# Kernel optimization log

Hardware: AMD Instinct MI355X
Metric: run time of the kernel (lower is better)

Reference implementation:

```python
import jax, jax.numpy as jnp
import numpy as np

N_NODES = 20000
N_EDGES = 320000
HIDDEN = 64
M = 8            # extra per-node sample axis implied by Linear2's (N, B, M) layout
IN_DIM = 1
OUT_DIM = 1
N_LAYERS = 5
BN_EPS = 1e-5


def setup_inputs() -> dict:
    key = jax.random.key(0)
    ks = jax.random.split(key, 10)
    x = jax.random.normal(ks[0], (N_NODES, IN_DIM, M), dtype=jnp.float32)
    edge_index = jax.random.randint(ks[1], (2, N_EDGES), 0, N_NODES, dtype=jnp.int64)
    batch = jnp.zeros((N_NODES,), dtype=jnp.int64)
    s = 0.1
    w1_0 = jax.random.normal(ks[2], (HIDDEN, IN_DIM), dtype=jnp.float32) * s
    w1 = jax.random.normal(ks[3], (N_LAYERS - 1, HIDDEN, HIDDEN), dtype=jnp.float32) * s
    b1 = jax.random.normal(ks[4], (N_LAYERS, HIDDEN), dtype=jnp.float32) * s
    w2 = jax.random.normal(ks[5], (N_LAYERS, HIDDEN, HIDDEN), dtype=jnp.float32) * s
    b2 = jax.random.normal(ks[6], (N_LAYERS, HIDDEN), dtype=jnp.float32) * s
    gamma = jnp.ones((N_LAYERS, HIDDEN), dtype=jnp.float32)
    beta = jnp.zeros((N_LAYERS, HIDDEN), dtype=jnp.float32)
    w_out = jax.random.normal(ks[7], (OUT_DIM, HIDDEN), dtype=jnp.float32) * s
    b_out = jnp.zeros((OUT_DIM,), dtype=jnp.float32)
    return {"x": x, "edge_index": edge_index, "batch": batch,
            "w1_0": w1_0, "w1": w1, "b1": b1, "w2": w2, "b2": b2,
            "gamma": gamma, "beta": beta, "w_out": w_out, "b_out": b_out}


def reference(x, edge_index, batch, w1_0, w1, b1, w2, b2, gamma, beta, w_out, b_out):
    src, dst = edge_index[0], edge_index[1]
    n = x.shape[0]
    h = x  # [N, C, M]
    for i in range(N_LAYERS):
        # GINConv (eps=0): nn(x + sum of neighbor features scattered by dst)
        agg = jax.ops.segment_sum(h[src], dst, num_segments=n)
        z = h + agg
        W1 = w1_0 if i == 0 else w1[i - 1]
        # Linear2 applies the linear over the channel axis (axis 1)
        z = jnp.einsum('ncm,oc->nom', z, W1) + b1[i][None, :, None]
        z = jax.nn.relu(z)
        z = jnp.einsum('ncm,oc->nom', z, w2[i]) + b2[i][None, :, None]
        z = jax.nn.relu(z)
        # BatchNorm1d over (N, C, M): per-channel stats over N and M (training-mode batch stats)
        mean = z.mean(axis=(0, 2), keepdims=True)
        var = z.var(axis=(0, 2), keepdims=True)
        z = (z - mean) * jax.lax.rsqrt(var + BN_EPS)
        z = z * gamma[i][None, :, None] + beta[i][None, :, None]
        # Dropout(0.5) treated as identity (eval behavior, deterministic reference)
        h = z
    # global mean pool with batch of all zeros -> single graph
    pooled = h.mean(axis=0, keepdims=True)          # [1, H, M]
    pooled = jnp.transpose(pooled, (0, 2, 1))        # [1, M, H]
    out = jax.nn.sigmoid(jnp.einsum('bmh,oh->bmo', pooled, w_out) + b_out)
    return out  # [1, M, OUT_DIM]
```

## Files before the change

### kernel.cpp

```cpp
#include <hip/hip_runtime.h>

#define N_NODES 20000
#define N_EDGES 320000
#define HID 64
#define MDIM 8
#define ROW 512
#define NM 160000.0f
#define NCHUNK 79
#define NSHADOW 16
#define ZSTRIDE 72

typedef unsigned int uint;
typedef unsigned char uchar;
typedef unsigned short ushort;
typedef __attribute__((ext_vector_type(8))) short bf16x8;
typedef __attribute__((ext_vector_type(4))) float f32x4;
typedef __attribute__((ext_vector_type(2))) float f32x2;

union U4B8 { uint4 u; bf16x8 b; };

__device__ __forceinline__ float bflo(uint u) { return __uint_as_float(u << 16); }
__device__ __forceinline__ float bfhi(uint u) { return __uint_as_float(u & 0xffff0000u); }
__device__ __forceinline__ uint f2bf(float f) {
    uint u = __float_as_uint(f);
    return (u + 0x7fffu + ((u >> 16) & 1u)) >> 16;
}
__device__ __forceinline__ uint pack2(float lo, float hi) { return f2bf(lo) | (f2bf(hi) << 16); }
__device__ __forceinline__ uint2 pkfp8(uint4 pk) {
    int lo = 0, hi = 0;
    lo = __builtin_amdgcn_cvt_pk_fp8_f32(bflo(pk.x), bfhi(pk.x), lo, false);
    lo = __builtin_amdgcn_cvt_pk_fp8_f32(bflo(pk.y), bfhi(pk.y), lo, true);
    hi = __builtin_amdgcn_cvt_pk_fp8_f32(bflo(pk.z), bfhi(pk.z), hi, false);
    hi = __builtin_amdgcn_cvt_pk_fp8_f32(bflo(pk.w), bfhi(pk.w), hi, true);
    uint2 r; r.x = (uint)lo; r.y = (uint)hi; return r;
}

__global__ __launch_bounds__(256) void k_hist(const int* __restrict__ dst, int* __restrict__ deg) {
    int e = blockIdx.x * 256 + threadIdx.x;
    if (e < N_EDGES) atomicAdd(&deg[dst[e]], 1);
}

__global__ __launch_bounds__(256) void k_csum(const int* __restrict__ deg, int* __restrict__ csum) {
    __shared__ int r[256];
    int t = threadIdx.x, i = blockIdx.x * 256 + t;
    r[t] = (i < N_NODES) ? deg[i] : 0;
    __syncthreads();
    for (int s = 128; s > 0; s >>= 1) { if (t < s) r[t] += r[t + s]; __syncthreads(); }
    if (t == 0) csum[blockIdx.x] = r[0];
}

__global__ __launch_bounds__(128) void k_cscan(const int* __restrict__ csum, int* __restrict__ chunkoff) {
    __shared__ int s[128];
    int t = threadIdx.x;
    s[t] = (t < NCHUNK) ? csum[t] : 0;
    __syncthreads();
    if (t == 0) { int run = 0; for (int j = 0; j < NCHUNK; ++j) { int x = s[j]; s[j] = run; run += x; } }
    __syncthreads();
    if (t < NCHUNK) chunkoff[t] = s[t];
}

__global__ __launch_bounds__(256) void k_chunkscan(const int* __restrict__ deg, const int* __restrict__ chunkoff,
                                                   int* __restrict__ offs) {
    __shared__ int sd[256];
    int t = threadIdx.x, i = blockIdx.x * 256 + t;
    int v = (i < N_NODES) ? deg[i] : 0;
    sd[t] = v;
    __syncthreads();
    for (int off = 1; off < 256; off <<= 1) {
        int x = (t >= off) ? sd[t - off] : 0;
        __syncthreads();
        sd[t] += x;
        __syncthreads();
    }
    if (i < N_NODES) offs[i] = sd[t] - v + chunkoff[blockIdx.x];
}

__global__ __launch_bounds__(256) void k_fill(const int* __restrict__ src, const int* __restrict__ dst,
                                              const int* __restrict__ offs, int* __restrict__ cursor,
                                              int* __restrict__ esrc) {
    int e = blockIdx.x * 256 + threadIdx.x;
    if (e < N_EDGES) {
        int d = dst[e];
        int p = atomicAdd(&cursor[d], 1);
        esrc[offs[d] + p] = src[e];
    }
}

__global__ __launch_bounds__(256) void k_prep(const float* __restrict__ w1, const float* __restrict__ w2,
                                              uint4* __restrict__ wfrag) {
    int id = blockIdx.x * 256 + threadIdx.x;
    if (id >= 4608) return;
    const float* W;
    int s;
    if (id < 4096) {
        int layer = id >> 10;
        int rem = id & 1023;
        int which = rem >> 9;
        s = rem & 511;
        W = which ? &w2[(size_t)(layer + 1) * 4096] : &w1[(size_t)layer * 4096];
    } else {
        s = id - 4096;
        W = w2;
    }
    int f = s >> 6, l = s & 63;
    int o = (f >> 1) * 16 + (l & 15);
    int c0 = (f & 1) * 32 + (l >> 4) * 8;
    const float* p = &W[o * 64 + c0];
    uint4 a;
    a.x = pack2(p[0], p[1]); a.y = pack2(p[2], p[3]);
    a.z = pack2(p[4], p[5]); a.w = pack2(p[6], p[7]);
    wfrag[id] = a;
}

__global__ __launch_bounds__(256) void k_layer0(const float* __restrict__ x, const int* __restrict__ offs,
                                                const int* __restrict__ deg, const int* __restrict__ esrc,
                                                const float* __restrict__ W10, const float* __restrict__ B1,
                                                const uint4* __restrict__ w2f0, const float* __restrict__ B2,
                                                uchar* __restrict__ zout8, float* __restrict__ shadow) {
    __shared__ uint4 w2s[512];
    __shared__ __align__(16) ushort zbuf[128 * ZSTRIDE];
    int tid = threadIdx.x;
    for (int s2 = tid; s2 < 512; s2 += 256) w2s[s2] = w2f0[s2];
    __syncthreads();
    int w = tid >> 6, t = tid & 63;
    int n0 = blockIdx.x * 16 + w * 4;
    int g = t >> 3, m = t & 7;
    float zin0v[4];
    #pragma unroll
    for (int i = 0; i < 4; ++i) {
        int n = n0 + i;
        int off = offs[n], dg = deg[n];
        float acc = (t < 8) ? x[n * 8 + t] : 0.f;
        for (int base = 0; base < dg; base += 8) {
            int k = base + g;
            float v = 0.f;
            if (k < dg) { int nb = esrc[off + k]; v = x[(size_t)nb * 8 + m]; }
            acc += v;
        }
        acc += __shfl_xor(acc, 8);
        acc += __shfl_xor(acc, 16);
        acc += __shfl_xor(acc, 32);
        zin0v[i] = acc;
    }
    bf16x8 bfr[2][2];
    #pragma unroll
    for (int q2 = 0; q2 < 2; ++q2) {
        int kb = q2 * 32 + (t >> 4) * 8;
        float4 wA = *(const float4*)&W10[kb];
        float4 wB = *(const float4*)&W10[kb + 4];
        float4 bA = *(const float4*)&B1[kb];
        float4 bB = *(const float4*)&B1[kb + 4];
        #pragma unroll
        for (int tau = 0; tau < 2; ++tau) {
            float zv = zin0v[tau * 2 + ((t & 15) >> 3)];
            U4B8 u;
            u.u.x = pack2(fmaxf(fmaf(wA.x, zv, bA.x), 0.f), fmaxf(fmaf(wA.y, zv, bA.y), 0.f));
            u.u.y = pack2(fmaxf(fmaf(wA.z, zv, bA.z), 0.f), fmaxf(fmaf(wA.w, zv, bA.w), 0.f));
            u.u.z = pack2(fmaxf(fmaf(wB.x, zv, bB.x), 0.f), fmaxf(fmaf(wB.y, zv, bB.y), 0.f));
            u.u.w = pack2(fmaxf(fmaf(wB.z, zv, bB.z), 0.f), fmaxf(fmaf(wB.w, zv, bB.w), 0.f));
            bfr[q2][tau] = u.b;
        }
    }
    f32x4 acc[4][2];
    #pragma unroll
    for (int o4 = 0; o4 < 4; ++o4) {
        float4 bv = *(const float4*)&B2[o4 * 16 + (t >> 4) * 4];
        #pragma unroll
        for (int tau = 0; tau < 2; ++tau) acc[o4][tau] = (f32x4){bv.x, bv.y, bv.z, bv.w};
    }
    #pragma unroll
    for (int o4 = 0; o4 < 4; ++o4)
        #pragma unroll
        for (int q2 = 0; q2 < 2; ++q2) {
            U4B8 a; a.u = w2s[(o4 * 2 + q2) * 64 + t];
            #pragma unroll
            for (int tau = 0; tau < 2; ++tau)
                acc[o4][tau] = __builtin_amdgcn_mfma_f32_16x16x32_bf16(a.b, bfr[q2][tau], acc[o4][tau], 0, 0, 0);
        }
    #pragma unroll
    for (int o4 = 0; o4 < 4; ++o4)
        #pragma unroll
        for (int tau = 0; tau < 2; ++tau) {
            acc[o4][tau][0] = fmaxf(acc[o4][tau][0], 0.f);
            acc[o4][tau][1] = fmaxf(acc[o4][tau][1], 0.f);
            acc[o4][tau][2] = fmaxf(acc[o4][tau][2], 0.f);
            acc[o4][tau][3] = fmaxf(acc[o4][tau][3], 0.f);
        }
    int sid = (blockIdx.x & (NSHADOW - 1)) * 128;
    #pragma unroll
    for (int o4 = 0; o4 < 4; ++o4)
        #pragma unroll
        for (int r = 0; r < 4; ++r) {
            float x0 = acc[o4][0][r], x1 = acc[o4][1][r];
            float sv = x0 + x1;
            float ssv = x0 * x0 + x1 * x1;
            sv += __shfl_xor(sv, 1);  ssv += __shfl_xor(ssv, 1);
            sv += __shfl_xor(sv, 2);  ssv += __shfl_xor(ssv, 2);
            sv += __shfl_xor(sv, 4);  ssv += __shfl_xor(ssv, 4);
            sv += __shfl_xor(sv, 8);  ssv += __shfl_xor(ssv, 8);
            if ((t & 15) == o4 * 4 + r) {
                int ch = o4 * 16 + (t >> 4) * 4 + r;
                atomicAdd(&shadow[sid + ch], sv);
                atomicAdd(&shadow[sid + 64 + ch], ssv);
            }
        }
    #pragma unroll
    for (int o4 = 0; o4 < 4; ++o4)
        #pragma unroll
        for (int tau = 0; tau < 2; ++tau) {
            uint* p = (uint*)&zbuf[(w * 32 + tau * 16 + (t & 15)) * ZSTRIDE + o4 * 16 + (t >> 4) * 4];
            p[0] = pack2(acc[o4][tau][0], acc[o4][tau][1]);
            p[1] = pack2(acc[o4][tau][2], acc[o4][tau][3]);
        }
    #pragma unroll
    for (int i = 0; i < 4; ++i) {
        uint4 pk = *(const uint4*)&zbuf[(w * 32 + i * 8 + (t >> 3)) * ZSTRIDE + (t & 7) * 8];
        ((uint2*)(zout8 + (size_t)(n0 + i) * ROW))[t] = pkfp8(pk);
    }
}

#define PAIRLD(rr, jj) do { \
    int nb_l = __builtin_amdgcn_readlane(idx, (jj)); \
    int nb_h = __builtin_amdgcn_readlane(idx, (jj) + 1); \
    int nb_ = hi ? nb_h : nb_l; \
    rr = ((const uint4*)(zprev8 + (size_t)nb_ * ROW))[q]; \
} while (0)

#define ACC16(rr) do { \
    f32x2 p_; \
    p_ = __builtin_amdgcn_cvt_pk_f32_fp8((int)rr.x, false); s0  += p_.x; s1  += p_.y; \
    p_ = __builtin_amdgcn_cvt_pk_f32_fp8((int)rr.x, true);  s2  += p_.x; s3  += p_.y; \
    p_ = __builtin_amdgcn_cvt_pk_f32_fp8((int)rr.y, false); s4  += p_.x; s5  += p_.y; \
    p_ = __builtin_amdgcn_cvt_pk_f32_fp8((int)rr.y, true);  s6  += p_.x; s7  += p_.y; \
    p_ = __builtin_amdgcn_cvt_pk_f32_fp8((int)rr.z, false); s8  += p_.x; s9  += p_.y; \
    p_ = __builtin_amdgcn_cvt_pk_f32_fp8((int)rr.z, true);  s10 += p_.x; s11 += p_.y; \
    p_ = __builtin_amdgcn_cvt_pk_f32_fp8((int)rr.w, false); s12 += p_.x; s13 += p_.y; \
    p_ = __builtin_amdgcn_cvt_pk_f32_fp8((int)rr.w, true);  s14 += p_.x; s15 += p_.y; \
} while (0)

__global__ __launch_bounds__(256) void k_layer(const uchar* __restrict__ zprev8,
                                               const float* __restrict__ shadow_prev,
                                               const float* __restrict__ gammaP, const float* __restrict__ betaP,
                                               const int* __restrict__ offs, const int* __restrict__ deg,
                                               const int* __restrict__ esrc,
                                               const uint4* __restrict__ w1f, const float* __restrict__ B1,
                                               const uint4* __restrict__ w2f, const float* __restrict__ B2,
                                               uchar* __restrict__ zout8, float* __restrict__ shadow) {
    __shared__ __align__(16) ushort zbuf[128 * ZSTRIDE];
    __shared__ float red[128];
    __shared__ __align__(16) float abl[128];
    int tid = threadIdx.x;
    int w = tid >> 6, t = tid & 63;
    int n0 = blockIdx.x * 16 + w * 4;
    int q = t & 31;
    int hi = t >> 5;
    int offv[4], dgv[4], idxv[4];
    #pragma unroll
    for (int i = 0; i < 4; ++i) { offv[i] = offs[n0 + i]; dgv[i] = deg[n0 + i]; }
    #pragma unroll
    for (int i = 0; i < 4; ++i) idxv[i] = (t < dgv[i]) ? esrc[offv[i] + t] : 0;
    if (tid < 128) {
        float s = 0.f;
        #pragma unroll
        for (int j = 0; j < NSHADOW; ++j) s += shadow_prev[j * 128 + tid];
        red[tid] = s;
    }
    __syncthreads();
    if (tid < 64) {
        float mean = red[tid] * (1.f / NM);
        float var = red[64 + tid] * (1.f / NM) - mean * mean;
        float a = gammaP[tid] * rsqrtf(var + 1e-5f);
        abl[tid] = a;
        abl[64 + tid] = betaP[tid] - mean * a;
    }
    __syncthreads();
    const float4* abp = (const float4*)abl;
    #pragma unroll
    for (int i = 0; i < 4; ++i) {
        int n = n0 + i;
        int off = offv[i], dg = dgv[i];
        float s0 = 0.f, s1 = 0.f, s2 = 0.f, s3 = 0.f, s4 = 0.f, s5 = 0.f, s6 = 0.f, s7 = 0.f;
        float s8 = 0.f, s9 = 0.f, s10 = 0.f, s11 = 0.f, s12 = 0.f, s13 = 0.f, s14 = 0.f, s15 = 0.f;
        for (int base = 0; base < dg; base += 64) {
            int cnt = dg - base; if (cnt > 64) cnt = 64;
            int idx = base ? ((t < cnt) ? esrc[off + base + t] : 0) : idxv[i];
            int j = 0;
            for (; j + 7 < cnt; j += 8) {
                uint4 r0, r1, r2, r3;
                PAIRLD(r0, j); PAIRLD(r1, j + 2); PAIRLD(r2, j + 4); PAIRLD(r3, j + 6);
                ACC16(r0); ACC16(r1); ACC16(r2); ACC16(r3);
            }
            for (; j + 1 < cnt; j += 2) {
                uint4 r0;
                PAIRLD(r0, j);
                ACC16(r0);
            }
            if (j < cnt) {
                int nb = __builtin_amdgcn_readlane(idx, j);
                if (!hi) {
                    uint4 r0 = ((const uint4*)(zprev8 + (size_t)nb * ROW))[q];
                    ACC16(r0);
                }
            }
        }
        float u, r0, r1, r2, r3, r4, r5, r6, r7;
        u = hi ? s0 : s8;   r0 = (hi ? s8  : s0) + __shfl_xor(u, 32);
        u = hi ? s1 : s9;   r1 = (hi ? s9  : s1) + __shfl_xor(u, 32);
        u = hi ? s2 : s10;  r2 = (hi ? s10 : s2) + __shfl_xor(u, 32);
        u = hi ? s3 : s11;  r3 = (hi ? s11 : s3) + __shfl_xor(u, 32);
        u = hi ? s4 : s12;  r4 = (hi ? s12 : s4) + __shfl_xor(u, 32);
        u = hi ? s5 : s13;  r5 = (hi ? s13 : s5) + __shfl_xor(u, 32);
        u = hi ? s6 : s14;  r6 = (hi ? s14 : s6) + __shfl_xor(u, 32);
        u = hi ? s7 : s15;  r7 = (hi ? s15 : s7) + __shfl_xor(u, 32);
        {
            uint2 sv = ((const uint2*)(zprev8 + (size_t)n * ROW))[q * 2 + hi];
            f32x2 p_;
            p_ = __builtin_amdgcn_cvt_pk_f32_fp8((int)sv.x, false); r0 += p_.x; r1 += p_.y;
            p_ = __builtin_amdgcn_cvt_pk_f32_fp8((int)sv.x, true);  r2 += p_.x; r3 += p_.y;
            p_ = __builtin_amdgcn_cvt_pk_f32_fp8((int)sv.y, false); r4 += p_.x; r5 += p_.y;
            p_ = __builtin_amdgcn_cvt_pk_f32_fp8((int)sv.y, true);  r6 += p_.x; r7 += p_.y;
        }
        int c4 = (q & 3) * 4 + hi * 2;
        float4 Af0 = abp[c4], Af1 = abp[c4 + 1];
        float4 Bf0 = abp[16 + c4], Bf1 = abp[16 + c4 + 1];
        float dp1 = (float)(dg + 1);
        uint4 pk;
        pk.x = pack2(fmaf(Af0.x, r0, Bf0.x * dp1), fmaf(Af0.y, r1, Bf0.y * dp1));
        pk.y = pack2(fmaf(Af0.z, r2, Bf0.z * dp1), fmaf(Af0.w, r3, Bf0.w * dp1));
        pk.z = pack2(fmaf(Af1.x, r4, Bf1.x * dp1), fmaf(Af1.y, r5, Bf1.y * dp1));
        pk.w = pack2(fmaf(Af1.z, r6, Bf1.z * dp1), fmaf(Af1.w, r7, Bf1.w * dp1));
        *(uint4*)&zbuf[(w * 32 + i * 8 + (q >> 2)) * ZSTRIDE + (q & 3) * 16 + hi * 8] = pk;
    }
    bf16x8 bfr[2][2];
    #pragma unroll
    for (int tau = 0; tau < 2; ++tau)
        #pragma unroll
        for (int q2 = 0; q2 < 2; ++q2) {
            U4B8 u;
            u.u = *(const uint4*)&zbuf[(w * 32 + tau * 16 + (t & 15)) * ZSTRIDE + q2 * 32 + (t >> 4) * 8];
            bfr[q2][tau] = u.b;
        }
    f32x4 acc[4][2];
    #pragma unroll
    for (int o4 = 0; o4 < 4; ++o4) {
        float4 bv = *(const float4*)&B1[o4 * 16 + (t >> 4) * 4];
        #pragma unroll
        for (int tau = 0; tau < 2; ++tau) acc[o4][tau] = (f32x4){bv.x, bv.y, bv.z, bv.w};
    }
    #pragma unroll
    for (int o4 = 0; o4 < 4; ++o4)
        #pragma unroll
        for (int q2 = 0; q2 < 2; ++q2) {
            U4B8 a; a.u = w1f[(o4 * 2 + q2) * 64 + t];
            #pragma unroll
            for (int tau = 0; tau < 2; ++tau)
                acc[o4][tau] = __builtin_amdgcn_mfma_f32_16x16x32_bf16(a.b, bfr[q2][tau], acc[o4][tau], 0, 0, 0);
        }
    #pragma unroll
    for (int o4 = 0; o4 < 4; ++o4)
        #pragma unroll
        for (int tau = 0; tau < 2; ++tau) {
            f32x4 v = acc[o4][tau];
            float h0 = fmaxf(v[0], 0.f), h1 = fmaxf(v[1], 0.f), h2 = fmaxf(v[2], 0.f), h3 = fmaxf(v[3], 0.f);
            uint* p = (uint*)&zbuf[(w * 32 + tau * 16 + (t & 15)) * ZSTRIDE + o4 * 16 + (t >> 4) * 4];
            p[0] = pack2(h0, h1); p[1] = pack2(h2, h3);
        }
    #pragma unroll
    for (int tau = 0; tau < 2; ++tau)
        #pragma unroll
        for (int q2 = 0; q2 < 2; ++q2) {
            U4B8 u;
            u.u = *(const uint4*)&zbuf[(w * 32 + tau * 16 + (t & 15)) * ZSTRIDE + q2 * 32 + (t >> 4) * 8];
            bfr[q2][tau] = u.b;
        }
    #pragma unroll
    for (int o4 = 0; o4 < 4; ++o4) {
        float4 bv = *(const float4*)&B2[o4 * 16 + (t >> 4) * 4];
        #pragma unroll
        for (int tau = 0; tau < 2; ++tau) acc[o4][tau] = (f32x4){bv.x, bv.y, bv.z, bv.w};
    }
    #pragma unroll
    for (int o4 = 0; o4 < 4; ++o4)
        #pragma unroll
        for (int q2 = 0; q2 < 2; ++q2) {
            U4B8 a; a.u = w2f[(o4 * 2 + q2) * 64 + t];
            #pragma unroll
            for (int tau = 0; tau < 2; ++tau)
                acc[o4][tau] = __builtin_amdgcn_mfma_f32_16x16x32_bf16(a.b, bfr[q2][tau], acc[o4][tau], 0, 0, 0);
        }
    #pragma unroll
    for (int o4 = 0; o4 < 4; ++o4)
        #pragma unroll
        for (int tau = 0; tau < 2; ++tau) {
            acc[o4][tau][0] = fmaxf(acc[o4][tau][0], 0.f);
            acc[o4][tau][1] = fmaxf(acc[o4][tau][1], 0.f);
            acc[o4][tau][2] = fmaxf(acc[o4][tau][2], 0.f);
            acc[o4][tau][3] = fmaxf(acc[o4][tau][3], 0.f);
        }
    int sid = (blockIdx.x & (NSHADOW - 1)) * 128;
    #pragma unroll
    for (int o4 = 0; o4 < 4; ++o4)
        #pragma unroll
        for (int r = 0; r < 4; ++r) {
            float x0 = acc[o4][0][r], x1 = acc[o4][1][r];
            float sv = x0 + x1;
            float ssv = x0 * x0 + x1 * x1;
            sv += __shfl_xor(sv, 1);  ssv += __shfl_xor(ssv, 1);
            sv += __shfl_xor(sv, 2);  ssv += __shfl_xor(ssv, 2);
            sv += __shfl_xor(sv, 4);  ssv += __shfl_xor(ssv, 4);
            sv += __shfl_xor(sv, 8);  ssv += __shfl_xor(ssv, 8);
            if ((t & 15) == o4 * 4 + r) {
                int ch = o4 * 16 + (t >> 4) * 4 + r;
                atomicAdd(&shadow[sid + ch], sv);
                atomicAdd(&shadow[sid + 64 + ch], ssv);
            }
        }
    #pragma unroll
    for (int o4 = 0; o4 < 4; ++o4)
        #pragma unroll
        for (int tau = 0; tau < 2; ++tau) {
            uint* p = (uint*)&zbuf[(w * 32 + tau * 16 + (t & 15)) * ZSTRIDE + o4 * 16 + (t >> 4) * 4];
            p[0] = pack2(acc[o4][tau][0], acc[o4][tau][1]);
            p[1] = pack2(acc[o4][tau][2], acc[o4][tau][3]);
        }
    #pragma unroll
    for (int i = 0; i < 4; ++i) {
        uint4 pk = *(const uint4*)&zbuf[(w * 32 + i * 8 + (t >> 3)) * ZSTRIDE + (t & 7) * 8];
        ((uint2*)(zout8 + (size_t)(n0 + i) * ROW))[t] = pkfp8(pk);
    }
}

__global__ __launch_bounds__(256) void k_pool(const uint* __restrict__ z8, float* __restrict__ pool) {
    int t = blockIdx.x * 256 + threadIdx.x;
    float s0 = 0.f, s1 = 0.f, s2 = 0.f, s3 = 0.f;
    for (int u = t; u < N_NODES * ROW / 4; u += 65536) {
        uint v = z8[u];
        f32x2 p0 = __builtin_amdgcn_cvt_pk_f32_fp8((int)v, false);
        f32x2 p1 = __builtin_amdgcn_cvt_pk_f32_fp8((int)v, true);
        s0 += p0.x; s1 += p0.y; s2 += p1.x; s3 += p1.y;
    }
    int k4 = t & 127;
    atomicAdd(&pool[k4 * 4 + 0], s0);
    atomicAdd(&pool[k4 * 4 + 1], s1);
    atomicAdd(&pool[k4 * 4 + 2], s2);
    atomicAdd(&pool[k4 * 4 + 3], s3);
}

__global__ __launch_bounds__(64) void k_out(const float* __restrict__ pool, const float* __restrict__ shadow4,
                                            const float* __restrict__ gamma4, const float* __restrict__ beta4,
                                            const float* __restrict__ wout, const float* __restrict__ bout,
                                            float* __restrict__ out) {
    int c = threadIdx.x;
    float s = 0.f, ss = 0.f;
    #pragma unroll
    for (int j = 0; j < NSHADOW; ++j) { s += shadow4[j * 128 + c]; ss += shadow4[j * 128 + 64 + c]; }
    float mean = s * (1.f / NM);
    float var = ss * (1.f / NM) - mean * mean;
    float a = gamma4[c] * rsqrtf(var + 1e-5f);
    float b = beta4[c] - mean * a;
    float wv = wout[c];
    for (int m = 0; m < 8; ++m) {
        float v = wv * (a * pool[m * 64 + c] * (1.f / N_NODES) + b);
        for (int off = 32; off > 0; off >>= 1) v += __shfl_down(v, off);
        if (c == 0) out[m] = 1.f / (1.f + expf(-(v + bout[0])));
    }
}

extern "C" void kernel_launch(void* const* d_in, const int* in_sizes, int n_in,
                              void* d_out, int out_size, void* d_ws, size_t ws_size,
                              hipStream_t stream) {
    const float* x     = (const float*)d_in[0];
    const int*   ei    = (const int*)d_in[1];
    const int*   srcp  = ei;
    const int*   dstp  = ei + N_EDGES;
    const float* w1_0  = (const float*)d_in[3];
    const float* w1    = (const float*)d_in[4];
    const float* b1    = (const float*)d_in[5];
    const float* w2    = (const float*)d_in[6];
    const float* b2    = (const float*)d_in[7];
    const float* gamma = (const float*)d_in[8];
    const float* beta  = (const float*)d_in[9];
    const float* wout  = (const float*)d_in[10];
    const float* bout  = (const float*)d_in[11];
    float* out = (float*)d_out;

    char* ws = (char*)d_ws;
    size_t off = 0;
    auto alloc = [&](size_t bytes) -> void* {
        void* p = ws + off;
        off = (off + bytes + 255) & ~(size_t)255;
        return p;
    };
    uchar* zA8   = (uchar*)alloc((size_t)N_NODES * ROW);
    uchar* zB8   = (uchar*)alloc((size_t)N_NODES * ROW);
    uint4* wfrag = (uint4*)alloc(4608 * 16);
    int* deg      = (int*)alloc(N_NODES * 4);
    int* cursor   = (int*)alloc(N_NODES * 4);
    float* shadow = (float*)alloc(5 * NSHADOW * 128 * 4);
    float* pool   = (float*)alloc(512 * 4);
    size_t zero_bytes = (size_t)((char*)pool - (char*)deg) + 512 * 4;
    int* offs     = (int*)alloc(N_NODES * 4);
    int* esrc     = (int*)alloc(N_EDGES * 4);
    int* csum     = (int*)alloc(NCHUNK * 4);
    int* chunkoff = (int*)alloc(NCHUNK * 4);

    hipMemsetAsync(deg, 0, zero_bytes, stream);

    k_hist<<<(N_EDGES + 255) / 256, 256, 0, stream>>>(dstp, deg);
    k_csum<<<NCHUNK, 256, 0, stream>>>(deg, csum);
    k_cscan<<<1, 128, 0, stream>>>(csum, chunkoff);
    k_chunkscan<<<NCHUNK, 256, 0, stream>>>(deg, chunkoff, offs);
    k_fill<<<(N_EDGES + 255) / 256, 256, 0, stream>>>(srcp, dstp, offs, cursor, esrc);
    k_prep<<<18, 256, 0, stream>>>(w1, w2, wfrag);

    k_layer0<<<N_NODES / 16, 256, 0, stream>>>(x, offs, deg, esrc, w1_0, b1, wfrag + 4096, b2,
                                               zA8, shadow);

    const uchar* zin8 = zA8;
    uchar* zo8 = zB8;
    for (int i = 1; i <= 4; ++i) {
        k_layer<<<N_NODES / 16, 256, 0, stream>>>(zin8,
                                                  shadow + (size_t)(i - 1) * NSHADOW * 128,
                                                  gamma + (i - 1) * 64, beta + (i - 1) * 64,
                                                  offs, deg, esrc,
                                                  wfrag + (size_t)(i - 1) * 1024, b1 + i * 64,
                                                  wfrag + (size_t)(i - 1) * 1024 + 512, b2 + i * 64,
                                                  zo8,
                                                  shadow + (size_t)i * NSHADOW * 128);
        const uchar* t8 = zin8; zin8 = zo8; zo8 = (uchar*)t8;
    }

    k_pool<<<256, 256, 0, stream>>>((const uint*)zA8, pool);
    k_out<<<1, 64, 0, stream>>>(pool, shadow + 4 * NSHADOW * 128, gamma + 256, beta + 256, wout, bout, out);
}
```

Measured before the change: 492.6 us.

## Pad CSR neighbor lists to multiples of 16 with zero node; single-wave layer blocks

Each node's CSR segment is padded to a multiple of 16 entries filled with a dummy zero-row node, so the gather loop runs in fixed 16-neighbor steps with no remainder paths. k_layer also becomes a 64-thread single-wave block with four nodes per block, and the self-row load is hoisted to the start of the kernel. The aim is to remove tail branching and raise the number of independent loads in flight. In exchange the kernel does up to 15 extra dummy gathers per node (about 50% more with an average degree of 16), needs an extra padding kernel and memsets, and recomputes the BN statistics in every small block.

```diff
diff --git a/kernel.cpp b/kernel.cpp
--- a/kernel.cpp
+++ b/kernel.cpp
@@ -9,6 +9,8 @@
 #define NCHUNK 79
 #define NSHADOW 16
 #define ZSTRIDE 72
+#define ZERO_NODE N_NODES
+#define ESRC_CAP 640000
 
 typedef unsigned int uint;
 typedef unsigned char uchar;
@@ -43,7 +45,7 @@
 __global__ __launch_bounds__(256) void k_csum(const int* __restrict__ deg, int* __restrict__ csum) {
     __shared__ int r[256];
     int t = threadIdx.x, i = blockIdx.x * 256 + t;
-    r[t] = (i < N_NODES) ? deg[i] : 0;
+    r[t] = (i < N_NODES) ? ((deg[i] + 15) & ~15) : 0;
     __syncthreads();
     for (int s = 128; s > 0; s >>= 1) { if (t < s) r[t] += r[t + s]; __syncthreads(); }
     if (t == 0) csum[blockIdx.x] = r[0];
@@ -63,7 +65,7 @@
                                                    int* __restrict__ offs) {
     __shared__ int sd[256];
     int t = threadIdx.x, i = blockIdx.x * 256 + t;
-    int v = (i < N_NODES) ? deg[i] : 0;
+    int v = (i < N_NODES) ? ((deg[i] + 15) & ~15) : 0;
     sd[t] = v;
     __syncthreads();
     for (int off = 1; off < 256; off <<= 1) {
@@ -84,6 +86,16 @@
         int p = atomicAdd(&cursor[d], 1);
         esrc[offs[d] + p] = src[e];
     }
+}
+
+__global__ __launch_bounds__(256) void k_pad(const int* __restrict__ deg, const int* __restrict__ offs,
+                                             int* __restrict__ esrc) {
+    int id = blockIdx.x * 256 + threadIdx.x;
+    if (id >= N_NODES * 16) return;
+    int n = id >> 4, s = id & 15;
+    int dg = deg[n], pdg = (dg + 15) & ~15;
+    int p = dg + s;
+    if (p < pdg) esrc[offs[n] + p] = ZERO_NODE;
 }
 
 __global__ __launch_bounds__(256) void k_prep(const float* __restrict__ w1, const float* __restrict__ w2,
@@ -238,69 +250,61 @@
     p_ = __builtin_amdgcn_cvt_pk_f32_fp8((int)rr.w, true);  s14 += p_.x; s15 += p_.y; \
 } while (0)
 
-__global__ __launch_bounds__(256) void k_layer(const uchar* __restrict__ zprev8,
-                                               const float* __restrict__ shadow_prev,
-                                               const float* __restrict__ gammaP, const float* __restrict__ betaP,
-                                               const int* __restrict__ offs, const int* __restrict__ deg,
-                                               const int* __restrict__ esrc,
-                                               const uint4* __restrict__ w1f, const float* __restrict__ B1,
-                                               const uint4* __restrict__ w2f, const float* __restrict__ B2,
-                                               uchar* __restrict__ zout8, float* __restrict__ shadow) {
-    __shared__ __align__(16) ushort zbuf[128 * ZSTRIDE];
-    __shared__ float red[128];
+__global__ __launch_bounds__(64, 4) void k_layer(const uchar* __restrict__ zprev8,
+                                                 const float* __restrict__ shadow_prev,
+                                                 const float* __restrict__ gammaP, const float* __restrict__ betaP,
+                                                 const int* __restrict__ offs, const int* __restrict__ deg,
+                                                 const int* __restrict__ esrc,
+                                                 const uint4* __restrict__ w1f, const float* __restrict__ B1,
+                                                 const uint4* __restrict__ w2f, const float* __restrict__ B2,
+                                                 uchar* __restrict__ zout8, float* __restrict__ shadow) {
+    __shared__ __align__(16) ushort zbuf[32 * ZSTRIDE];
     __shared__ __align__(16) float abl[128];
-    int tid = threadIdx.x;
-    int w = tid >> 6, t = tid & 63;
-    int n0 = blockIdx.x * 16 + w * 4;
+    int t = threadIdx.x;
+    int n0 = blockIdx.x * 4;
     int q = t & 31;
     int hi = t >> 5;
-    int offv[4], dgv[4], idxv[4];
-    #pragma unroll
-    for (int i = 0; i < 4; ++i) { offv[i] = offs[n0 + i]; dgv[i] = deg[n0 + i]; }
-    #pragma unroll
-    for (int i = 0; i < 4; ++i) idxv[i] = (t < dgv[i]) ? esrc[offv[i] + t] : 0;
-    if (tid < 128) {
-        float s = 0.f;
-        #pragma unroll
-        for (int j = 0; j < NSHADOW; ++j) s += shadow_prev[j * 128 + tid];
-        red[tid] = s;
-    }
-    __syncthreads();
-    if (tid < 64) {
-        float mean = red[tid] * (1.f / NM);
-        float var = red[64 + tid] * (1.f / NM) - mean * mean;
-        float a = gammaP[tid] * rsqrtf(var + 1e-5f);
-        abl[tid] = a;
-        abl[64 + tid] = betaP[tid] - mean * a;
+    int offv[4], dgv[4], pdgv[4], idxv[4];
+    uint2 selfv[4];
+    #pragma unroll
+    for (int i = 0; i < 4; ++i) {
+        offv[i] = offs[n0 + i];
+        dgv[i] = deg[n0 + i];
+        pdgv[i] = (dgv[i] + 15) & ~15;
+    }
+    #pragma unroll
+    for (int i = 0; i < 4; ++i) idxv[i] = (t < pdgv[i]) ? esrc[offv[i] + t] : 0;
+    #pragma unroll
+    for (int i = 0; i < 4; ++i) selfv[i] = ((const uint2*)(zprev8 + (size_t)(n0 + i) * ROW))[q * 2 + hi];
+    {
+        float s = 0.f, ss = 0.f;
+        #pragma unroll
+        for (int j = 0; j < NSHADOW; ++j) {
+            s  += shadow_prev[j * 128 + t];
+            ss += shadow_prev[j * 128 + 64 + t];
+        }
+        float mean = s * (1.f / NM);
+        float var = ss * (1.f / NM) - mean * mean;
+        float a = gammaP[t] * rsqrtf(var + 1e-5f);
+        abl[t] = a;
+        abl[64 + t] = betaP[t] - mean * a;
     }
     __syncthreads();
     const float4* abp = (const float4*)abl;
     #pragma unroll
     for (int i = 0; i < 4; ++i) {
-        int n = n0 + i;
-        int off = offv[i], dg = dgv[i];
+        int off = offv[i], dg = dgv[i], pdg = pdgv[i];
         float s0 = 0.f, s1 = 0.f, s2 = 0.f, s3 = 0.f, s4 = 0.f, s5 = 0.f, s6 = 0.f, s7 = 0.f;
         float s8 = 0.f, s9 = 0.f, s10 = 0.f, s11 = 0.f, s12 = 0.f, s13 = 0.f, s14 = 0.f, s15 = 0.f;
-        for (int base = 0; base < dg; base += 64) {
-            int cnt = dg - base; if (cnt > 64) cnt = 64;
+        for (int base = 0; base < pdg; base += 64) {
+            int cnt = pdg - base; if (cnt > 64) cnt = 64;
             int idx = base ? ((t < cnt) ? esrc[off + base + t] : 0) : idxv[i];
-            int j = 0;
-            for (; j + 7 < cnt; j += 8) {
-                uint4 r0, r1, r2, r3;
-                PAIRLD(r0, j); PAIRLD(r1, j + 2); PAIRLD(r2, j + 4); PAIRLD(r3, j + 6);
+            for (int j = 0; j < cnt; j += 16) {
+                uint4 r0, r1, r2, r3, r4, r5, r6, r7;
+                PAIRLD(r0, j);      PAIRLD(r1, j + 2);  PAIRLD(r2, j + 4);  PAIRLD(r3, j + 6);
+                PAIRLD(r4, j + 8);  PAIRLD(r5, j + 10); PAIRLD(r6, j + 12); PAIRLD(r7, j + 14);
                 ACC16(r0); ACC16(r1); ACC16(r2); ACC16(r3);
-            }
-            for (; j + 1 < cnt; j += 2) {
-                uint4 r0;
-                PAIRLD(r0, j);
-                ACC16(r0);
-            }
-            if (j < cnt) {
-                int nb = __builtin_amdgcn_readlane(idx, j);
-                if (!hi) {
-                    uint4 r0 = ((const uint4*)(zprev8 + (size_t)nb * ROW))[q];
-                    ACC16(r0);
-                }
+                ACC16(r4); ACC16(r5); ACC16(r6); ACC16(r7);
             }
         }
         float u, r0, r1, r2, r3, r4, r5, r6, r7;
@@ -313,7 +317,7 @@
         u = hi ? s6 : s14;  r6 = (hi ? s14 : s6) + __shfl_xor(u, 32);
         u = hi ? s7 : s15;  r7 = (hi ? s15 : s7) + __shfl_xor(u, 32);
         {
-            uint2 sv = ((const uint2*)(zprev8 + (size_t)n * ROW))[q * 2 + hi];
+            uint2 sv = selfv[i];
             f32x2 p_;
             p_ = __builtin_amdgcn_cvt_pk_f32_fp8((int)sv.x, false); r0 += p_.x; r1 += p_.y;
             p_ = __builtin_amdgcn_cvt_pk_f32_fp8((int)sv.x, true);  r2 += p_.x; r3 += p_.y;
@@ -329,7 +333,7 @@
         pk.y = pack2(fmaf(Af0.z, r2, Bf0.z * dp1), fmaf(Af0.w, r3, Bf0.w * dp1));
         pk.z = pack2(fmaf(Af1.x, r4, Bf1.x * dp1), fmaf(Af1.y, r5, Bf1.y * dp1));
         pk.w = pack2(fmaf(Af1.z, r6, Bf1.z * dp1), fmaf(Af1.w, r7, Bf1.w * dp1));
-        *(uint4*)&zbuf[(w * 32 + i * 8 + (q >> 2)) * ZSTRIDE + (q & 3) * 16 + hi * 8] = pk;
+        *(uint4*)&zbuf[(i * 8 + (q >> 2)) * ZSTRIDE + (q & 3) * 16 + hi * 8] = pk;
     }
     bf16x8 bfr[2][2];
     #pragma unroll
@@ -337,7 +341,7 @@
         #pragma unroll
         for (int q2 = 0; q2 < 2; ++q2) {
             U4B8 u;
-            u.u = *(const uint4*)&zbuf[(w * 32 + tau * 16 + (t & 15)) * ZSTRIDE + q2 * 32 + (t >> 4) * 8];
+            u.u = *(const uint4*)&zbuf[(tau * 16 + (t & 15)) * ZSTRIDE + q2 * 32 + (t >> 4) * 8];
             bfr[q2][tau] = u.b;
         }
     f32x4 acc[4][2];
@@ -362,7 +366,7 @@
         for (int tau = 0; tau < 2; ++tau) {
             f32x4 v = acc[o4][tau];
             float h0 = fmaxf(v[0], 0.f), h1 = fmaxf(v[1], 0.f), h2 = fmaxf(v[2], 0.f), h3 = fmaxf(v[3], 0.f);
-            uint* p = (uint*)&zbuf[(w * 32 + tau * 16 + (t & 15)) * ZSTRIDE + o4 * 16 + (t >> 4) * 4];
+            uint* p = (uint*)&zbuf[(tau * 16 + (t & 15)) * ZSTRIDE + o4 * 16 + (t >> 4) * 4];
             p[0] = pack2(h0, h1); p[1] = pack2(h2, h3);
         }
     #pragma unroll
@@ -370,7 +374,7 @@
         #pragma unroll
         for (int q2 = 0; q2 < 2; ++q2) {
             U4B8 u;
-            u.u = *(const uint4*)&zbuf[(w * 32 + tau * 16 + (t & 15)) * ZSTRIDE + q2 * 32 + (t >> 4) * 8];
+            u.u = *(const uint4*)&zbuf[(tau * 16 + (t & 15)) * ZSTRIDE + q2 * 32 + (t >> 4) * 8];
             bfr[q2][tau] = u.b;
         }
     #pragma unroll
@@ -419,13 +423,13 @@
     for (int o4 = 0; o4 < 4; ++o4)
         #pragma unroll
         for (int tau = 0; tau < 2; ++tau) {
-            uint* p = (uint*)&zbuf[(w * 32 + tau * 16 + (t & 15)) * ZSTRIDE + o4 * 16 + (t >> 4) * 4];
+            uint* p = (uint*)&zbuf[(tau * 16 + (t & 15)) * ZSTRIDE + o4 * 16 + (t >> 4) * 4];
             p[0] = pack2(acc[o4][tau][0], acc[o4][tau][1]);
             p[1] = pack2(acc[o4][tau][2], acc[o4][tau][3]);
         }
     #pragma unroll
     for (int i = 0; i < 4; ++i) {
-        uint4 pk = *(const uint4*)&zbuf[(w * 32 + i * 8 + (t >> 3)) * ZSTRIDE + (t & 7) * 8];
+        uint4 pk = *(const uint4*)&zbuf[(i * 8 + (t >> 3)) * ZSTRIDE + (t & 7) * 8];
         ((uint2*)(zout8 + (size_t)(n0 + i) * ROW))[t] = pkfp8(pk);
     }
 }
@@ -491,8 +495,8 @@
         off = (off + bytes + 255) & ~(size_t)255;
         return p;
     };
-    uchar* zA8   = (uchar*)alloc((size_t)N_NODES * ROW);
-    uchar* zB8   = (uchar*)alloc((size_t)N_NODES * ROW);
+    uchar* zA8   = (uchar*)alloc((size_t)(N_NODES + 1) * ROW);
+    uchar* zB8   = (uchar*)alloc((size_t)(N_NODES + 1) * ROW);
     uint4* wfrag = (uint4*)alloc(4608 * 16);
     int* deg      = (int*)alloc(N_NODES * 4);
     int* cursor   = (int*)alloc(N_NODES * 4);
@@ -500,17 +504,20 @@
     float* pool   = (float*)alloc(512 * 4);
     size_t zero_bytes = (size_t)((char*)pool - (char*)deg) + 512 * 4;
     int* offs     = (int*)alloc(N_NODES * 4);
-    int* esrc     = (int*)alloc(N_EDGES * 4);
+    int* esrc     = (int*)alloc(ESRC_CAP * 4);
     int* csum     = (int*)alloc(NCHUNK * 4);
     int* chunkoff = (int*)alloc(NCHUNK * 4);
 
     hipMemsetAsync(deg, 0, zero_bytes, stream);
+    hipMemsetAsync(zA8 + (size_t)N_NODES * ROW, 0, ROW, stream);
+    hipMemsetAsync(zB8 + (size_t)N_NODES * ROW, 0, ROW, stream);
 
     k_hist<<<(N_EDGES + 255) / 256, 256, 0, stream>>>(dstp, deg);
     k_csum<<<NCHUNK, 256, 0, stream>>>(deg, csum);
     k_cscan<<<1, 128, 0, stream>>>(csum, chunkoff);
     k_chunkscan<<<NCHUNK, 256, 0, stream>>>(deg, chunkoff, offs);
     k_fill<<<(N_EDGES + 255) / 256, 256, 0, stream>>>(srcp, dstp, offs, cursor, esrc);
+    k_pad<<<(N_NODES * 16 + 255) / 256, 256, 0, stream>>>(deg, offs, esrc);
     k_prep<<<18, 256, 0, stream>>>(w1, w2, wfrag);
 
     k_layer0<<<N_NODES / 16, 256, 0, stream>>>(x, offs, deg, esrc, w1_0, b1, wfrag + 4096, b2,
@@ -519,14 +526,14 @@
     const uchar* zin8 = zA8;
     uchar* zo8 = zB8;
     for (int i = 1; i <= 4; ++i) {
-        k_layer<<<N_NODES / 16, 256, 0, stream>>>(zin8,
-                                                  shadow + (size_t)(i - 1) * NSHADOW * 128,
-                                                  gamma + (i - 1) * 64, beta + (i - 1) * 64,
-                                                  offs, deg, esrc,
-                                                  wfrag + (size_t)(i - 1) * 1024, b1 + i * 64,
-                                                  wfrag + (size_t)(i - 1) * 1024 + 512, b2 + i * 64,
-                                                  zo8,
-                                                  shadow + (size_t)i * NSHADOW * 128);
+        k_layer<<<N_NODES / 4, 64, 0, stream>>>(zin8,
+                                                shadow + (size_t)(i - 1) * NSHADOW * 128,
+                                                gamma + (i - 1) * 64, beta + (i - 1) * 64,
+                                                offs, deg, esrc,
+                                                wfrag + (size_t)(i - 1) * 1024, b1 + i * 64,
+                                                wfrag + (size_t)(i - 1) * 1024 + 512, b2 + i * 64,
+                                                zo8,
+                                                shadow + (size_t)i * NSHADOW * 128);
         const uchar* t8 = zin8; zin8 = zo8; zo8 = (uchar*)t8;
     }
 
```

Measured after the change: 734.3 us. 49.1% more time.
